# Kernel optimization log

Hardware: AMD Instinct MI355X
Metric: run time of the kernel (lower is better)

## Reference

```python
import jax, jax.numpy as jnp
import numpy as np

B, T, H = 8192, 1024, 8


def setup_inputs() -> dict:
    key = jax.random.key(0)
    ks = jax.random.split(key, 7)
    bound_rnn = 1.0 / np.sqrt(H)
    bound_fc = 1.0 / np.sqrt(H)
    x = jax.random.normal(ks[0], (B, T), dtype=jnp.float32)
    W_ih = jax.random.uniform(ks[1], (H, 1), minval=-bound_rnn, maxval=bound_rnn, dtype=jnp.float32)
    W_hh = jax.random.uniform(ks[2], (H, H), minval=-bound_rnn, maxval=bound_rnn, dtype=jnp.float32)
    b_ih = jax.random.uniform(ks[3], (H,), minval=-bound_rnn, maxval=bound_rnn, dtype=jnp.float32)
    b_hh = jax.random.uniform(ks[4], (H,), minval=-bound_rnn, maxval=bound_rnn, dtype=jnp.float32)
    W_fc = jax.random.uniform(ks[5], (1, H), minval=-bound_fc, maxval=bound_fc, dtype=jnp.float32)
    b_fc = jax.random.uniform(ks[6], (1,), minval=-bound_fc, maxval=bound_fc, dtype=jnp.float32)
    return {"x": x, "W_ih": W_ih, "W_hh": W_hh, "b_ih": b_ih, "b_hh": b_hh,
            "W_fc": W_fc, "b_fc": b_fc}


def reference(x, W_ih, W_hh, b_ih, b_hh, W_fc, b_fc):
    # x: [B, T] -> unsqueeze(-1) -> [B, T, 1]; input_size == 1 so
    # x_t @ W_ih^T == x_t * W_ih[:, 0]. Precompute input projection once.
    pre = x[:, :, None] * W_ih[:, 0] + (b_ih + b_hh)  # [B, T, H]
    pre_t = jnp.swapaxes(pre, 0, 1)                   # [T, B, H]

    def step(h, p_t):
        h = jnp.tanh(p_t + h @ W_hh.T)                # [B, H]
        return h, None

    h0 = jnp.zeros((x.shape[0], W_hh.shape[0]), dtype=x.dtype)
    h_last, _ = jax.lax.scan(step, h0, pre_t)
    return jax.nn.sigmoid(h_last @ W_fc.T + b_fc)     # [B, 1]
```

## Files before the change

### kernel.cpp

```cpp
#include <hip/hip_runtime.h>


#define T_LEN 1024
#define DPP_XOR1 0xB1
#define DPP_XOR2 0x4E
#define DPP_XOR7 0x141
#define K_2LN2 2.8853900817779268f

template <int CTRL>
__device__ __forceinline__ float fdpp(float v) {
    int i = __builtin_bit_cast(int, v);
    int r = __builtin_amdgcn_mov_dpp(i, CTRL, 0xF, 0xF, true);
    return __builtin_bit_cast(float, r);
}

__device__ __forceinline__ float fast_sigmoid(float z) {
    float e = __builtin_amdgcn_exp2f(z * -1.4426950408889634f);
    return __builtin_amdgcn_rcpf(1.0f + e);
}

#define STEP(PRE)                                                              \
    asm volatile(                                                              \
        "v_fma_f32 %[u], %[r], %[w0], %[p]\n\t"                                \
        "v_mov_b32_dpp %[m7], %[r] row_half_mirror row_mask:0xf bank_mask:0xf\n\t" \
        "v_fmac_f32_dpp %[u], %[r], %[w1] quad_perm:[1,0,3,2] row_mask:0xf bank_mask:0xf\n\t" \
        "v_fmac_f32_dpp %[u], %[r], %[w2] quad_perm:[2,3,0,1] row_mask:0xf bank_mask:0xf\n\t" \
        "v_fmac_f32_dpp %[u], %[r], %[w3] quad_perm:[3,2,1,0] row_mask:0xf bank_mask:0xf\n\t" \
        "v_fmac_f32 %[u], %[m7], %[w7]\n\t"                                    \
        "v_fmac_f32_dpp %[u], %[m7], %[w4] quad_perm:[3,2,1,0] row_mask:0xf bank_mask:0xf\n\t" \
        "v_fmac_f32_dpp %[u], %[m7], %[w5] quad_perm:[2,3,0,1] row_mask:0xf bank_mask:0xf\n\t" \
        "v_fmac_f32_dpp %[u], %[m7], %[w6] quad_perm:[1,0,3,2] row_mask:0xf bank_mask:0xf\n\t" \
        "v_exp_f32 %[e], %[u]\n\t"                                             \
        "s_nop 1\n\t"                                                          \
        "v_add_f32 %[u], 1.0, %[e]\n\t"                                        \
        "v_rcp_f32 %[r], %[u]\n\t"                                             \
        "s_nop 1\n\t"                                                          \
        : [r]"+v"(r), [u]"=&v"(u_t), [e]"=&v"(e_t), [m7]"=&v"(m7_t)            \
        : [p]"v"(PRE), [w0]"v"(wq0), [w1]"v"(wq1), [w2]"v"(wq2),               \
          [w3]"v"(wq3), [w4]"v"(wq4), [w5]"v"(wq5), [w6]"v"(wq6),              \
          [w7]"v"(wq7))

__global__ __launch_bounds__(256) void rnn_oct_asm_kernel(
    const float* __restrict__ x, const float* __restrict__ W_ih,
    const float* __restrict__ W_hh, const float* __restrict__ b_ih,
    const float* __restrict__ b_hh, const float* __restrict__ W_fc,
    const float* __restrict__ b_fc, float* __restrict__ out, int B)
{
    const int tid = blockIdx.x * 256 + threadIdx.x;
    const int j = tid & 7;
    const int b = tid >> 3;
    if (b >= B) return;

    float wv0 = W_hh[j * 8 + (j ^ 0)];
    float wv1 = W_hh[j * 8 + (j ^ 1)];
    float wv2 = W_hh[j * 8 + (j ^ 2)];
    float wv3 = W_hh[j * 8 + (j ^ 3)];
    float wv4 = W_hh[j * 8 + (j ^ 4)];
    float wv5 = W_hh[j * 8 + (j ^ 5)];
    float wv6 = W_hh[j * 8 + (j ^ 6)];
    float wv7 = W_hh[j * 8 + (j ^ 7)];
    float rowsum = ((wv0 + wv1) + (wv2 + wv3)) + ((wv4 + wv5) + (wv6 + wv7));
    const float wq0 = -2.0f * K_2LN2 * wv0;
    const float wq1 = -2.0f * K_2LN2 * wv1;
    const float wq2 = -2.0f * K_2LN2 * wv2;
    const float wq3 = -2.0f * K_2LN2 * wv3;
    const float wq4 = -2.0f * K_2LN2 * wv4;
    const float wq5 = -2.0f * K_2LN2 * wv5;
    const float wq6 = -2.0f * K_2LN2 * wv6;
    const float wq7 = -2.0f * K_2LN2 * wv7;
    const float biasp = K_2LN2 * (b_ih[j] + b_hh[j] + rowsum);
    const float wihp  = K_2LN2 * W_ih[j];

    const float wfc = W_fc[j];
    float sw = wfc;
    sw += fdpp<DPP_XOR1>(sw);
    sw += fdpp<DPP_XOR2>(sw);
    sw += fdpp<DPP_XOR7>(sw);
    const float cfc  = b_fc[0] + sw;
    const float wfc2 = -2.0f * wfc;

    const float* xb = x + (size_t)b * T_LEN;
    float r = 0.5f;
    float u_t, e_t, m7_t;

    float4 A0 = *(const float4*)(xb + 0);
    float4 A1 = *(const float4*)(xb + 4);
    float4 A2 = *(const float4*)(xb + 8);
    float4 A3 = *(const float4*)(xb + 12);

#pragma unroll 1
    for (int t0 = 0; t0 < T_LEN; t0 += 16) {
        float pre[16];
        pre[0]  = __builtin_fmaf(A0.x, wihp, biasp);
        pre[1]  = __builtin_fmaf(A0.y, wihp, biasp);
        pre[2]  = __builtin_fmaf(A0.z, wihp, biasp);
        pre[3]  = __builtin_fmaf(A0.w, wihp, biasp);
        pre[4]  = __builtin_fmaf(A1.x, wihp, biasp);
        pre[5]  = __builtin_fmaf(A1.y, wihp, biasp);
        pre[6]  = __builtin_fmaf(A1.z, wihp, biasp);
        pre[7]  = __builtin_fmaf(A1.w, wihp, biasp);
        pre[8]  = __builtin_fmaf(A2.x, wihp, biasp);
        pre[9]  = __builtin_fmaf(A2.y, wihp, biasp);
        pre[10] = __builtin_fmaf(A2.z, wihp, biasp);
        pre[11] = __builtin_fmaf(A2.w, wihp, biasp);
        pre[12] = __builtin_fmaf(A3.x, wihp, biasp);
        pre[13] = __builtin_fmaf(A3.y, wihp, biasp);
        pre[14] = __builtin_fmaf(A3.z, wihp, biasp);
        pre[15] = __builtin_fmaf(A3.w, wihp, biasp);

        if (t0 + 16 < T_LEN) {
            A0 = *(const float4*)(xb + t0 + 16);
            A1 = *(const float4*)(xb + t0 + 20);
            A2 = *(const float4*)(xb + t0 + 24);
            A3 = *(const float4*)(xb + t0 + 28);
        }

#pragma unroll
        for (int i = 0; i < 16; ++i)
            STEP(pre[i]);
    }

    float sv = r * wfc2;
    sv += fdpp<DPP_XOR1>(sv);
    sv += fdpp<DPP_XOR2>(sv);
    sv += fdpp<DPP_XOR7>(sv);
    if (j == 0) out[b] = fast_sigmoid(sv + cfc);
}

extern "C" void kernel_launch(void* const* d_in, const int* in_sizes, int n_in,
                              void* d_out, int out_size, void* d_ws, size_t ws_size,
                              hipStream_t stream) {
    const float* x    = (const float*)d_in[0];
    const float* W_ih = (const float*)d_in[1];
    const float* W_hh = (const float*)d_in[2];
    const float* b_ih = (const float*)d_in[3];
    const float* b_hh = (const float*)d_in[4];
    const float* W_fc = (const float*)d_in[5];
    const float* b_fc = (const float*)d_in[6];
    float* out = (float*)d_out;

    const int B = in_sizes[0] / T_LEN;
    const int threads = B * 8;
    const int grid = threads / 256;
    rnn_oct_asm_kernel<<<grid, 256, 0, stream>>>(x, W_ih, W_hh, b_ih, b_hh, W_fc, b_fc, out, B);
}
```

Measured before the change: 47.52 us.

## Fuse input projection into step asm and double-buffer x loads

The per-step input projection FMA moves into the inline asm step, where it fills the latency slot after v_exp that previously held an s_nop. A rotating 4-entry pre buffer computes values two steps ahead. The x loads are double-buffered across two 16-element register sets with a 32-step loop body, so loads have a full half-iteration of latency hiding. At the end the loads wrap to offset 0 and fetch unused data, which costs a little redundant traffic and some extra registers.

Measured after the change: 43.90 us. 1.08x faster.

```diff
diff --git a/kernel.cpp b/kernel.cpp
--- a/kernel.cpp
+++ b/kernel.cpp
@@ -19,9 +19,9 @@
     return __builtin_amdgcn_rcpf(1.0f + e);
 }
 
-#define STEP(PRE)                                                              \
+#define STEP(PUSE, PDEF, X)                                                    \
     asm volatile(                                                              \
-        "v_fma_f32 %[u], %[r], %[w0], %[p]\n\t"                                \
+        "v_fma_f32 %[u], %[r], %[w0], %[pu]\n\t"                               \
         "v_mov_b32_dpp %[m7], %[r] row_half_mirror row_mask:0xf bank_mask:0xf\n\t" \
         "v_fmac_f32_dpp %[u], %[r], %[w1] quad_perm:[1,0,3,2] row_mask:0xf bank_mask:0xf\n\t" \
         "v_fmac_f32_dpp %[u], %[r], %[w2] quad_perm:[2,3,0,1] row_mask:0xf bank_mask:0xf\n\t" \
@@ -31,16 +31,18 @@
         "v_fmac_f32_dpp %[u], %[m7], %[w5] quad_perm:[2,3,0,1] row_mask:0xf bank_mask:0xf\n\t" \
         "v_fmac_f32_dpp %[u], %[m7], %[w6] quad_perm:[1,0,3,2] row_mask:0xf bank_mask:0xf\n\t" \
         "v_exp_f32 %[e], %[u]\n\t"                                             \
-        "s_nop 1\n\t"                                                          \
+        "v_fma_f32 %[pd], %[x], %[wih], %[bs]\n\t"                             \
+        "s_nop 0\n\t"                                                          \
         "v_add_f32 %[u], 1.0, %[e]\n\t"                                        \
         "v_rcp_f32 %[r], %[u]\n\t"                                             \
         "s_nop 1\n\t"                                                          \
-        : [r]"+v"(r), [u]"=&v"(u_t), [e]"=&v"(e_t), [m7]"=&v"(m7_t)            \
-        : [p]"v"(PRE), [w0]"v"(wq0), [w1]"v"(wq1), [w2]"v"(wq2),               \
-          [w3]"v"(wq3), [w4]"v"(wq4), [w5]"v"(wq5), [w6]"v"(wq6),              \
-          [w7]"v"(wq7))
+        : [r]"+v"(r), [u]"=&v"(u_t), [e]"=&v"(e_t), [m7]"=&v"(m7_t),           \
+          [pd]"=&v"(PDEF)                                                      \
+        : [pu]"v"(PUSE), [x]"v"(X), [wih]"v"(wihp), [bs]"v"(biasp),            \
+          [w0]"v"(wq0), [w1]"v"(wq1), [w2]"v"(wq2), [w3]"v"(wq3),              \
+          [w4]"v"(wq4), [w5]"v"(wq5), [w6]"v"(wq6), [w7]"v"(wq7))
 
-__global__ __launch_bounds__(256) void rnn_oct_asm_kernel(
+__global__ __launch_bounds__(256) void rnn_oct_asm3_kernel(
     const float* __restrict__ x, const float* __restrict__ W_ih,
     const float* __restrict__ W_hh, const float* __restrict__ b_ih,
     const float* __restrict__ b_hh, const float* __restrict__ W_fc,
@@ -87,37 +89,64 @@
     float4 A1 = *(const float4*)(xb + 4);
     float4 A2 = *(const float4*)(xb + 8);
     float4 A3 = *(const float4*)(xb + 12);
+    float4 B0 = *(const float4*)(xb + 16);
+    float4 B1 = *(const float4*)(xb + 20);
+    float4 B2 = *(const float4*)(xb + 24);
+    float4 B3 = *(const float4*)(xb + 28);
+
+    float pre[4];
+    pre[0] = __builtin_fmaf(A0.x, wihp, biasp);
+    pre[1] = __builtin_fmaf(A0.y, wihp, biasp);
 
 #pragma unroll 1
-    for (int t0 = 0; t0 < T_LEN; t0 += 16) {
-        float pre[16];
-        pre[0]  = __builtin_fmaf(A0.x, wihp, biasp);
-        pre[1]  = __builtin_fmaf(A0.y, wihp, biasp);
-        pre[2]  = __builtin_fmaf(A0.z, wihp, biasp);
-        pre[3]  = __builtin_fmaf(A0.w, wihp, biasp);
-        pre[4]  = __builtin_fmaf(A1.x, wihp, biasp);
-        pre[5]  = __builtin_fmaf(A1.y, wihp, biasp);
-        pre[6]  = __builtin_fmaf(A1.z, wihp, biasp);
-        pre[7]  = __builtin_fmaf(A1.w, wihp, biasp);
-        pre[8]  = __builtin_fmaf(A2.x, wihp, biasp);
-        pre[9]  = __builtin_fmaf(A2.y, wihp, biasp);
-        pre[10] = __builtin_fmaf(A2.z, wihp, biasp);
-        pre[11] = __builtin_fmaf(A2.w, wihp, biasp);
-        pre[12] = __builtin_fmaf(A3.x, wihp, biasp);
-        pre[13] = __builtin_fmaf(A3.y, wihp, biasp);
-        pre[14] = __builtin_fmaf(A3.z, wihp, biasp);
-        pre[15] = __builtin_fmaf(A3.w, wihp, biasp);
+    for (int t0 = 0; t0 < T_LEN; t0 += 32) {
+        STEP(pre[0], pre[2], A0.z);
+        STEP(pre[1], pre[3], A0.w);
+        STEP(pre[2], pre[0], A1.x);
+        STEP(pre[3], pre[1], A1.y);
+        STEP(pre[0], pre[2], A1.z);
+        STEP(pre[1], pre[3], A1.w);
+        STEP(pre[2], pre[0], A2.x);
+        STEP(pre[3], pre[1], A2.y);
+        STEP(pre[0], pre[2], A2.z);
+        STEP(pre[1], pre[3], A2.w);
+        STEP(pre[2], pre[0], A3.x);
+        STEP(pre[3], pre[1], A3.y);
+        STEP(pre[0], pre[2], A3.z);
+        STEP(pre[1], pre[3], A3.w);
+        STEP(pre[2], pre[0], B0.x);
+        STEP(pre[3], pre[1], B0.y);
 
-        if (t0 + 16 < T_LEN) {
-            A0 = *(const float4*)(xb + t0 + 16);
-            A1 = *(const float4*)(xb + t0 + 20);
-            A2 = *(const float4*)(xb + t0 + 24);
-            A3 = *(const float4*)(xb + t0 + 28);
+        {
+            int offA = t0 + 32;
+            if (offA > T_LEN - 16) offA = 0;
+            const float4* pA = (const float4*)(xb + offA);
+            A0 = pA[0]; A1 = pA[1]; A2 = pA[2]; A3 = pA[3];
         }
 
-#pragma unroll
-        for (int i = 0; i < 16; ++i)
-            STEP(pre[i]);
+        STEP(pre[0], pre[2], B0.z);
+        STEP(pre[1], pre[3], B0.w);
+        STEP(pre[2], pre[0], B1.x);
+        STEP(pre[3], pre[1], B1.y);
+        STEP(pre[0], pre[2], B1.z);
+        STEP(pre[1], pre[3], B1.w);
+        STEP(pre[2], pre[0], B2.x);
+        STEP(pre[3], pre[1], B2.y);
+        STEP(pre[0], pre[2], B2.z);
+        STEP(pre[1], pre[3], B2.w);
+        STEP(pre[2], pre[0], B3.x);
+        STEP(pre[3], pre[1], B3.y);
+        STEP(pre[0], pre[2], B3.z);
+        STEP(pre[1], pre[3], B3.w);
+        STEP(pre[2], pre[0], A0.x);
+        STEP(pre[3], pre[1], A0.y);
+
+        {
+            int offB = t0 + 48;
+            if (offB > T_LEN - 16) offB = 0;
+            const float4* pB = (const float4*)(xb + offB);
+            B0 = pB[0]; B1 = pB[1]; B2 = pB[2]; B3 = pB[3];
+        }
     }
 
     float sv = r * wfc2;
@@ -142,5 +171,5 @@
     const int B = in_sizes[0] / T_LEN;
     const int threads = B * 8;
     const int grid = threads / 256;
-    rnn_oct_asm_kernel<<<grid, 256, 0, stream>>>(x, W_ih, W_hh, b_ih, b_hh, W_fc, b_fc, out, B);
+    rnn_oct_asm3_kernel<<<grid, 256, 0, stream>>>(x, W_ih, W_hh, b_ih, b_hh, W_fc, b_fc, out, B);
 }
```
